# Optimization experiments

Measured on AMD Instinct MI355X. Metric: run time of the kernel, lower is better.

Reference implementation:

```python
import jax, jax.numpy as jnp
import numpy as np

CURVS = (-1.0, 0.0, 1.0, -0.5)
N, E, B = 50000, 800000, 128
IN, HID, OUT, GHID = 128, 128, 128, 32
K = len(CURVS)
TAU_MIN, TAU_MAX = 0.05, 10.0
EPS = 1e-15


def _vnorm(x):
    return jnp.maximum(jnp.linalg.norm(x, axis=-1, keepdims=True), EPS)


def tan_k(x, k):
    if k > 0:
        sk = np.sqrt(k)
        return jnp.tan(x * sk) / sk
    if k < 0:
        sk = np.sqrt(-k)
        return jnp.tanh(x * sk) / sk
    return x


def artan_k(x, k):
    if k > 0:
        sk = np.sqrt(k)
        return jnp.arctan(x * sk) / sk
    if k < 0:
        sk = np.sqrt(-k)
        return jnp.arctanh(jnp.clip(x * sk, -1.0 + 1e-7, 1.0 - 1e-7)) / sk
    return x


def project(x, k):
    # clip inside Poincare ball for k<0; identity otherwise (geoopt Stereographic.projx)
    if k < 0:
        maxn = (1.0 - 1e-5) / np.sqrt(-k)
        n = _vnorm(x)
        return jnp.where(n > maxn, x * (maxn / n), x)
    return x


def expmap0(u, k):
    n = _vnorm(u)
    return project(tan_k(n, k) * u / n, k)


def logmap0(y, k):
    n = _vnorm(y)
    return artan_k(n, k) * y / n


def mobius_add(x, y, k):
    x2 = jnp.sum(x * x, -1, keepdims=True)
    y2 = jnp.sum(y * y, -1, keepdims=True)
    xy = jnp.sum(x * y, -1, keepdims=True)
    num = (1.0 - 2.0 * k * xy - k * y2) * x + (1.0 + k * x2) * y
    den = jnp.maximum(1.0 - 2.0 * k * xy + k * k * x2 * y2, 1e-15)
    return project(num / den, k)


def mobius_matvec(W, x, k):
    mx = x @ W.T
    if k == 0:
        return mx
    xn = _vnorm(x)
    mxn = _vnorm(mx)
    res = tan_k(mxn / xn * artan_k(xn, k), k) * mx / mxn
    res = jnp.where(jnp.sum(jnp.abs(mx), -1, keepdims=True) == 0.0, 0.0, res)
    return project(res, k)


def dist(x, y, k):
    return 2.0 * artan_k(_vnorm(mobius_add(-x, y, k)), k)[..., 0]


def setup_inputs():
    key = jax.random.key(0)
    ks = jax.random.split(key, 12)
    x = jax.random.normal(ks[0], (N, IN), jnp.float32)
    edge_index = jax.random.randint(ks[1], (2, E), 0, N)
    batch = jnp.sort(jax.random.randint(ks[2], (N,), 0, B))
    s1 = float(np.sqrt(2.0 / (IN + HID)))
    s2 = float(np.sqrt(2.0 / (HID + OUT)))
    sg1 = float(np.sqrt(2.0 / (IN + GHID)))
    sg2 = float(np.sqrt(2.0 / (GHID + OUT)))
    raw0 = float(np.log(np.expm1(1.0 - TAU_MIN)))
    return {
        "x": x,
        "edge_index": edge_index,
        "batch": batch,
        "expert_w1": jax.random.normal(ks[3], (K, HID, IN), jnp.float32) * s1,
        "expert_b1": jnp.zeros((K, HID), jnp.float32),
        "expert_w2": jax.random.normal(ks[4], (K, OUT, HID), jnp.float32) * s2,
        "expert_b2": jnp.zeros((K, OUT), jnp.float32),
        "gate_w1": jax.random.normal(ks[5], (GHID, IN), jnp.float32) * sg1,
        "gate_b1": jnp.zeros((GHID,), jnp.float32),
        "gate_w2": jax.random.normal(ks[6], (OUT, GHID), jnp.float32) * sg2,
        "gate_b2": jnp.zeros((OUT,), jnp.float32),
        "gate_u": jax.random.normal(ks[7], (K, OUT), jnp.float32) * 0.02,
        "tau_raw": jnp.full((K,), raw0, jnp.float32),
    }


def _graph_norm(edge_index):
    loops = jnp.arange(N)
    row = jnp.concatenate([edge_index[0], loops])
    col = jnp.concatenate([edge_index[1], loops])
    deg = jax.ops.segment_sum(jnp.ones(E + N, jnp.float32), col, num_segments=N)
    dinv = deg ** -0.5  # deg >= 1 due to self loops
    return row, col, dinv[row] * dinv[col]


def _kappa_conv(xm, W, b, row, col, enorm, k):
    h = mobius_matvec(W, xm, k)
    bias_pt = expmap0(b[None, :], k)  # proju at origin is identity
    h = mobius_add(h, bias_pt, k)
    t = logmap0(h, k)  # [N, out]
    agg = jax.ops.segment_sum(enorm[:, None] * t[row], col, num_segments=N)
    return expmap0(agg, k)


def reference(x, edge_index, batch, expert_w1, expert_b1, expert_w2, expert_b2,
              gate_w1, gate_b1, gate_w2, gate_b2, gate_u, tau_raw):
    x = x.astype(jnp.float32)
    row, col, enorm = _graph_norm(edge_index)
    counts = jnp.maximum(
        jax.ops.segment_sum(jnp.ones(N, jnp.float32), batch, num_segments=B), 1.0)[:, None]

    # --- Riemannian experts ---
    embs = []
    for i, kv in enumerate(CURVS):
        xm = expmap0(x, kv)  # manifold init (proju at origin = identity)
        xm = _kappa_conv(xm, expert_w1[i], expert_b1[i], row, col, enorm, kv)
        xm = _kappa_conv(xm, expert_w2[i], expert_b2[i], row, col, enorm, kv)
        z = logmap0(xm, kv)
        embs.append(jax.ops.segment_sum(z, batch, num_segments=B) / counts)
    features = jnp.concatenate(embs, axis=-1)  # [B, K*OUT]

    # --- Euclidean gating encoder (GCN) ---
    def gcn(h, W, b):
        m = (h @ W.T)
        out = jax.ops.segment_sum(enorm[:, None] * m[row], col, num_segments=N) + b
        return jax.nn.relu(out)

    g = gcn(x, gate_w1, gate_b1)
    g = gcn(g, gate_w2, gate_b2)
    hgate = jax.ops.segment_sum(g, batch, num_segments=B) / counts  # [B, OUT]

    # --- Geometric distance gate ---
    tau = jnp.clip(jax.nn.softplus(tau_raw) + TAU_MIN, TAU_MIN, TAU_MAX)
    dists = []
    for i, kv in enumerate(CURVS):
        zk = expmap0(hgate, kv)
        yk = expmap0(gate_u[i][None, :], kv)
        dists.append(dist(zk, yk, kv))
    dists = jnp.stack(dists, axis=-1)  # [B, K]
    weights = jax.nn.softmax(-dists / tau[None, :], axis=-1)

    scaled = features * jnp.repeat(weights, OUT, axis=1)
    return scaled, weights, dists, tau
```

## Files before the change

### kernel.cpp

```cpp
#include <hip/hip_runtime.h>
#include <math.h>

#define NN 50000
#define EE 800000
#define ETOT (EE + NN)
#define BB 128
#define DIM 128
#define GHID 32
#define CHUNK 128
#define NCHUNK ((ETOT + CHUNK - 1) / CHUNK)
#define SCB 196

typedef _Float16 f16;
typedef _Float16 f16x2 __attribute__((ext_vector_type(2)));
typedef _Float16 f16x8 __attribute__((ext_vector_type(8)));
typedef float f32x4 __attribute__((ext_vector_type(4)));

struct CurvPack {
  float k[4], sk[4], mx[4];
};

__device__ __forceinline__ float wsum64(float v) {
#pragma unroll
  for (int m = 32; m; m >>= 1) v += __shfl_xor(v, m, 64);
  return v;
}

__device__ __forceinline__ float tan_k_d(float x, float kv, float sk) {
  if (kv > 0.f) return tanf(x * sk) / sk;
  if (kv < 0.f) return tanhf(x * sk) / sk;
  return x;
}

__device__ __forceinline__ float artan_k_d(float x, float kv, float sk) {
  if (kv > 0.f) return atanf(x * sk) / sk;
  if (kv < 0.f) {
    float t = x * sk;
    t = fminf(fmaxf(t, -1.f + 1e-7f), 1.f - 1e-7f);
    return atanhf(t) / sk;
  }
  return x;
}

__device__ __forceinline__ float proj_scale_d(float n, float kv, float maxn) {
  if (kv < 0.f && n > maxn) return maxn / n;
  return 1.f;
}

__global__ void k_init(float* __restrict__ deg, int n) {
  int i = blockIdx.x * 256 + threadIdx.x;
  if (i < n) deg[i] = 1.0f;
}

__global__ void k_counts(const int* __restrict__ batch, int* __restrict__ boff,
                         float* __restrict__ counts, int n) {
  int b = threadIdx.x;
  if (b <= 128) {
    int lo = 0, hi = n;
    while (lo < hi) {
      int mid = (lo + hi) >> 1;
      if (batch[mid] < b) lo = mid + 1; else hi = mid;
    }
    boff[b] = lo;
  }
  __syncthreads();
  if (b < 128) counts[b] = (float)(boff[b + 1] - boff[b]);
}

__global__ void k_deg(const int* __restrict__ ei, float* __restrict__ deg, int e) {
  int i = blockIdx.x * 256 + threadIdx.x;
  if (i < e) atomicAdd(&deg[ei[e + i]], 1.0f);
}

__global__ void k_dinv(float* __restrict__ deg, int* __restrict__ ideg, int n) {
  int i = blockIdx.x * 256 + threadIdx.x;
  if (i < n) {
    float d = deg[i];
    ideg[i] = (int)(d + 0.5f);
    deg[i] = 1.0f / sqrtf(d);
  }
}

__global__ void k_scanA(const int* __restrict__ ideg, int* __restrict__ bsum, int n) {
  __shared__ int ls[4];
  int i = blockIdx.x * 256 + threadIdx.x;
  int v = (i < n) ? ideg[i] : 0;
#pragma unroll
  for (int m = 1; m < 64; m <<= 1) v += __shfl_xor(v, m, 64);
  if ((threadIdx.x & 63) == 0) ls[threadIdx.x >> 6] = v;
  __syncthreads();
  if (threadIdx.x == 0) bsum[blockIdx.x] = ls[0] + ls[1] + ls[2] + ls[3];
}

__global__ void k_scanB(int* __restrict__ bsum, int nb) {
  __shared__ int wsh[4];
  int tid = threadIdx.x;
  int lane = tid & 63, w = tid >> 6;
  int v = (tid < nb) ? bsum[tid] : 0;
  int x = v;
#pragma unroll
  for (int o = 1; o < 64; o <<= 1) {
    int t = __shfl_up(x, o, 64);
    if (lane >= o) x += t;
  }
  if (lane == 63) wsh[w] = x;
  __syncthreads();
  int add = 0;
  for (int k2 = 0; k2 < w; k2++) add += wsh[k2];
  if (tid < nb) bsum[tid] = add + x - v;
}

__global__ void k_scanC(const int* __restrict__ ideg, const int* __restrict__ bsum,
                        int* __restrict__ off, int* __restrict__ cursor, int n) {
  __shared__ int wsh[4];
  int i = blockIdx.x * 256 + threadIdx.x;
  int lane = threadIdx.x & 63, w = threadIdx.x >> 6;
  int v = (i < n) ? ideg[i] : 0;
  int x = v;
#pragma unroll
  for (int o = 1; o < 64; o <<= 1) {
    int t = __shfl_up(x, o, 64);
    if (lane >= o) x += t;
  }
  if (lane == 63) wsh[w] = x;
  __syncthreads();
  int add = bsum[blockIdx.x];
  for (int k2 = 0; k2 < w; k2++) add += wsh[k2];
  int excl = add + x - v;
  if (i < n) {
    off[i] = excl;
    cursor[i] = excl;
  }
  if (i == n - 1) off[n] = excl + v;
}

__global__ void k_bnodes(const int* __restrict__ off, int* __restrict__ bnode, int nchunk,
                         int n) {
  int g = blockIdx.x * 256 + threadIdx.x;
  if (g >= nchunk) return;
  int e0 = g * CHUNK;
  int lo = 0, hi = n;
  while (hi - lo > 1) {
    int mid = (lo + hi) >> 1;
    if (off[mid] <= e0) lo = mid; else hi = mid;
  }
  bnode[g] = lo;
}

__global__ void k_bslot(const int* __restrict__ bnode, int* __restrict__ bslot, int nchunk) {
  int g = blockIdx.x * 256 + threadIdx.x;
  if (g >= nchunk) return;
  int v = bnode[g];
  int lo = 0, hi = g;
  while (lo < hi) {
    int mid = (lo + hi) >> 1;
    if (bnode[mid] < v) lo = mid + 1; else hi = mid;
  }
  bslot[g] = lo;
}

__device__ __forceinline__ bool span_head(const int* bnode, const int* bslot, const int* off,
                                          int g, int& nd) {
  if (bslot[g] != g) return false;
  nd = bnode[g];
  int s = off[nd], e = off[nd + 1];
  return (s / CHUNK) != ((e - 1) / CHUNK);
}

__global__ void k_zeroc(const int* __restrict__ bnode, const int* __restrict__ bslot,
                        const int* __restrict__ off, float* __restrict__ aggc, int nchunk) {
  int g = blockIdx.x * 4 + (threadIdx.x >> 6);
  int lane = threadIdx.x & 63;
  if (g >= nchunk) return;
  int nd;
  if (!span_head(bnode, bslot, off, g, nd)) return;
  float2 z = make_float2(0.f, 0.f);
#pragma unroll
  for (int i = 0; i < 4; i++) ((float2*)aggc)[(size_t)g * 256 + i * 64 + lane] = z;
}

__global__ void k_place(const int* __restrict__ ei, const float* __restrict__ dinv,
                        int* __restrict__ cursor, int2* __restrict__ esw, int e, int n) {
  int i = blockIdx.x * 256 + threadIdx.x;
  int et = e + n;
  if (i >= et) return;
  int r_, c_;
  if (i < e) {
    r_ = ei[i];
    c_ = ei[e + i];
  } else {
    r_ = i - e;
    c_ = i - e;
  }
  int p = atomicAdd(&cursor[c_], 1);
  esw[p] = make_int2(r_, __float_as_int(dinv[r_] * dinv[c_]));
}

__global__ void k_nodeprep(const float* __restrict__ x, float* __restrict__ scl,
                           float* __restrict__ xnk, int n, CurvPack cp) {
  int wid = blockIdx.x * 4 + (threadIdx.x >> 6);
  int lane = threadIdx.x & 63;
  if (wid >= n) return;
  float2 v = ((const float2*)x)[(size_t)wid * 64 + lane];
  float n2 = wsum64(v.x * v.x + v.y * v.y);
  float nraw = sqrtf(n2);
  if (lane < 4) {
    float kv = cp.k[lane], sk = cp.sk[lane], maxn = cp.mx[lane];
    float nnv = fmaxf(nraw, 1e-15f);
    float tk = tan_k_d(nnv, kv, sk);
    float s = tk / nnv;
    float pn = fmaxf(fabsf(tk) * (nraw / nnv), 1e-15f);
    float ps = proj_scale_d(pn, kv, maxn);
    scl[(size_t)lane * n + wid] = s * ps;
    xnk[(size_t)lane * n + wid] = pn * ps;
  }
}

__global__ void k_biaspt_all(const float* __restrict__ eb1, const float* __restrict__ eb2,
                             float* __restrict__ biasb, CurvPack cp) {
  __shared__ float l2[2];
  int blk = blockIdx.x;
  int ex = blk >> 1, layer = blk & 1;
  float kv = cp.k[ex], sk = cp.sk[ex], maxn = cp.mx[ex];
  const float* b = (layer ? eb2 : eb1) + ex * 128;
  float* outb = biasb + blk * 132;
  int j = threadIdx.x;
  float v = b[j];
  float n2 = wsum64(v * v);
  if ((j & 63) == 0) l2[j >> 6] = n2;
  __syncthreads();
  n2 = l2[0] + l2[1];
  float nraw = sqrtf(n2);
  float nnv = fmaxf(nraw, 1e-15f);
  float tk = tan_k_d(nnv, kv, sk);
  float s = tk / nnv;
  float pn = fmaxf(fabsf(tk) * (nraw / nnv), 1e-15f);
  float ps = proj_scale_d(pn, kv, maxn);
  float bp = ps * s * v;
  outb[j] = bp;
  float y2v = wsum64(bp * bp);
  __syncthreads();
  if ((j & 63) == 0) l2[j >> 6] = y2v;
  __syncthreads();
  if (j == 0) outb[128] = l2[0] + l2[1];
}

__global__ void k_w2h(const float* __restrict__ ew1, const float* __restrict__ ew2,
                      f16* __restrict__ whi, f16* __restrict__ wlo) {
  int i = blockIdx.x * 256 + threadIdx.x;
  if (i >= 8 * 16384) return;
  int slot = i >> 14;
  int r = i & 16383;
  int ex = slot >> 1, layer = slot & 1;
  float w = (layer ? ew2 : ew1)[ex * 16384 + r];
  f16 h = (f16)w;
  whi[i] = h;
  wlo[i] = (f16)(w - (float)h);
}

__global__ __launch_bounds__(256) void k_matmfma(
    const float* __restrict__ A, int astr, int aoffPerEx, const float* __restrict__ sclB,
    const float* __restrict__ xnkB, const f16* __restrict__ whiB,
    const f16* __restrict__ wloB, const float* __restrict__ biasB, int layer,
    f16* __restrict__ tout, int n, CurvPack cp) {
  __shared__ float red[3][16][4];
  __shared__ float redT[16][4];
  __shared__ float nAs[16], nCs[16], nL[16];
  int ex = blockIdx.y;
  float kv = cp.k[ex], sk = cp.sk[ex], maxn = cp.mx[ex];
  const f16* whi = whiB + (size_t)(ex * 2 + layer) * 16384;
  const f16* wlo = wloB + (size_t)(ex * 2 + layer) * 16384;
  const float* biasb = biasB + (ex * 2 + layer) * 132;
  const float* scale = sclB + (size_t)ex * n;
  const float* xnorm = xnkB + (size_t)ex * n;

  int tid = threadIdx.x;
  int w = tid >> 6;
  int lane = tid & 63;
  int col = lane & 15;
  int quad = lane >> 4;
  int n0w = blockIdx.x * 16;
  if (n0w >= n) return;

  int anodec = min(n0w + col, n - 1);
  const float* arow = A + (size_t)anodec * astr + ex * aoffPerEx;
  int jt0 = w * 2;

  f32x4 acc[2];
  acc[0] = (f32x4){0.f, 0.f, 0.f, 0.f};
  acc[1] = (f32x4){0.f, 0.f, 0.f, 0.f};

#pragma unroll
  for (int kc = 0; kc < 4; kc++) {
    int kb = kc * 32 + quad * 8;
    float4 a0 = *(const float4*)(arow + kb);
    float4 a1 = *(const float4*)(arow + kb + 4);
    float av[8] = {a0.x, a0.y, a0.z, a0.w, a1.x, a1.y, a1.z, a1.w};
    f16x8 Ah, Al;
#pragma unroll
    for (int i = 0; i < 8; i++) {
      f16 h = (f16)av[i];
      Ah[i] = h;
      Al[i] = (f16)(av[i] - (float)h);
    }
#pragma unroll
    for (int j2 = 0; j2 < 2; j2++) {
      const f16* bh = whi + (size_t)((jt0 + j2) * 16 + col) * 128 + kb;
      const f16* bl = wlo + (size_t)((jt0 + j2) * 16 + col) * 128 + kb;
      f16x8 Bh = *(const f16x8*)bh;
      f16x8 Bl = *(const f16x8*)bl;
      acc[j2] = __builtin_amdgcn_mfma_f32_16x16x32_f16(Ah, Bh, acc[j2], 0, 0, 0);
      acc[j2] = __builtin_amdgcn_mfma_f32_16x16x32_f16(Ah, Bl, acc[j2], 0, 0, 0);
      acc[j2] = __builtin_amdgcn_mfma_f32_16x16x32_f16(Al, Bh, acc[j2], 0, 0, 0);
    }
  }

  float bpj[2];
  bpj[0] = biasb[jt0 * 16 + col];
  bpj[1] = biasb[(jt0 + 1) * 16 + col];
  float y2 = biasb[128];

#pragma unroll
  for (int r = 0; r < 4; r++) {
    float s0 = 0.f, s1 = 0.f, s2 = 0.f;
#pragma unroll
    for (int j2 = 0; j2 < 2; j2++) {
      float v = acc[j2][r];
      s0 = fmaf(v, v, s0);
      s1 += fabsf(v);
      s2 = fmaf(v, bpj[j2], s2);
    }
#pragma unroll
    for (int m = 1; m < 16; m <<= 1) {
      s0 += __shfl_xor(s0, m, 64);
      s1 += __shfl_xor(s1, m, 64);
      s2 += __shfl_xor(s2, m, 64);
    }
    if (col == 0) {
      red[0][quad * 4 + r][w] = s0;
      red[1][quad * 4 + r][w] = s1;
      red[2][quad * 4 + r][w] = s2;
    }
  }
  __syncthreads();

  if (tid < 16) {
    int gnode = min(n0w + tid, n - 1);
    float sc = scale[gnode];
    float s0f = (red[0][tid][0] + red[0][tid][1] + red[0][tid][2] + red[0][tid][3]) * sc * sc;
    float s1f = (red[1][tid][0] + red[1][tid][1] + red[1][tid][2] + red[1][tid][3]) * fabsf(sc);
    float s2f = (red[2][tid][0] + red[2][tid][1] + red[2][tid][2] + red[2][tid][3]) * sc;
    float xnr = xnorm[gnode];
    float xn = fmaxf(xnr, 1e-15f);
    float mxraw = sqrtf(s0f);
    float mxv = fmaxf(mxraw, 1e-15f);
    float ar = artan_k_d(xn, kv, sk);
    float c1 = tan_k_d(mxv / xn * ar, kv, sk);
    float s = (s1f == 0.f) ? 0.f : c1 / mxv;
    float pn = fmaxf(fabsf(c1) * (mxraw / mxv), 1e-15f);
    float ps = (s1f == 0.f) ? 1.f : proj_scale_d(pn, kv, maxn);
    s *= ps;
    float x2 = (s * s) * s0f;
    float xy = s * s2f;
    float Aa = 1.f - 2.f * kv * xy - kv * y2;
    float Cc = 1.f + kv * x2;
    float den = fmaxf(1.f - 2.f * kv * xy + (kv * kv) * x2 * y2, 1e-15f);
    nAs[tid] = Aa * s / den * sc;
    nCs[tid] = Cc / den;
  }
  __syncthreads();

#pragma unroll
  for (int r = 0; r < 4; r++) {
    int idx = quad * 4 + r;
    float Asc = nAs[idx], Cs = nCs[idx];
    float t0 = 0.f;
#pragma unroll
    for (int j2 = 0; j2 < 2; j2++) {
      float v = fmaf(Asc, acc[j2][r], Cs * bpj[j2]);
      t0 = fmaf(v, v, t0);
    }
#pragma unroll
    for (int m = 1; m < 16; m <<= 1) t0 += __shfl_xor(t0, m, 64);
    if (col == 0) redT[idx][w] = t0;
  }
  __syncthreads();

  if (tid < 16) {
    float t0f = redT[tid][0] + redT[tid][1] + redT[tid][2] + redT[tid][3];
    float nraw = sqrtf(t0f);
    float ps2 = proj_scale_d(fmaxf(nraw, 1e-15f), kv, maxn);
    float nh = fmaxf(ps2 * nraw, 1e-15f);
    nL[tid] = artan_k_d(nh, kv, sk) / nh * ps2;
  }
  __syncthreads();

#pragma unroll
  for (int r = 0; r < 4; r++) {
    int idx = quad * 4 + r;
    int gnode = n0w + idx;
    if (gnode >= n) continue;
    float Asc = nAs[idx], Cs = nCs[idx], L = nL[idx];
    f16* trow = tout + (size_t)gnode * 512 + ex * 128;
#pragma unroll
    for (int j2 = 0; j2 < 2; j2++) {
      float v = fmaf(Asc, acc[j2][r], Cs * bpj[j2]);
      trow[(jt0 + j2) * 16 + col] = (f16)(L * v);
    }
  }
}

template <int MODE, int NE>
__global__ __launch_bounds__(256) void k_aggF(
    const int2* __restrict__ esw, const int* __restrict__ off,
    const int* __restrict__ bnode, const int* __restrict__ bslot,
    const int* __restrict__ batch, const f16x2* __restrict__ t, float* __restrict__ agg1,
    float* __restrict__ aggc, float* __restrict__ scl2, float* __restrict__ xnk2,
    float* __restrict__ feats, const float* __restrict__ bias, float* __restrict__ hgate,
    int etot, int n, CurvPack cp) {
  int gw = blockIdx.x * 4 + (threadIdx.x >> 6);
  int lane = threadIdx.x & 63;
  int e0 = gw * CHUNK;
  if (e0 >= etot) return;
  int e1 = min(e0 + CHUNK, etot);
  int bnHead = bnode[gw];
  int slotA = bslot[gw];
  int slotB = ((gw + 1) * CHUNK < etot) ? bslot[gw + 1] : slotA;
  int cur = bnHead;
  int runStart = off[cur];
  int eend = off[cur + 1];
  float ax[NE], ay[NE], pax[NE], pay[NE];
#pragma unroll
  for (int e = 0; e < NE; e++) {
    ax[e] = ay[e] = pax[e] = pay[e] = 0.f;
  }
  int bcur = (MODE >= 1) ? batch[cur] : 0;
  float bbx = 0.f, bby = 0.f;
  if (MODE == 2) {
    float2 bb = ((const float2*)bias)[lane];
    bbx = bb.x;
    bby = bb.y;
  }

  auto flushInterior = [&]() {
#pragma unroll
    for (int e = 0; e < NE; e++) {
      if (MODE == 0) {
        ((float2*)agg1)[(size_t)cur * 256 + e * 64 + lane] = make_float2(ax[e], ay[e]);
        float n2 = wsum64(fmaf(ax[e], ax[e], ay[e] * ay[e]));
        float nraw = sqrtf(n2);
        float nnv = fmaxf(nraw, 1e-15f);
        float tk = tan_k_d(nnv, cp.k[e], cp.sk[e]);
        float s = tk / nnv;
        float pn = fmaxf(fabsf(tk) * (nraw / nnv), 1e-15f);
        float ps = proj_scale_d(pn, cp.k[e], cp.mx[e]);
        if (lane == 0) {
          scl2[(size_t)e * n + cur] = s * ps;
          xnk2[(size_t)e * n + cur] = pn * ps;
        }
      } else if (MODE == 1) {
        float n2 = wsum64(fmaf(ax[e], ax[e], ay[e] * ay[e]));
        float nraw = sqrtf(n2);
        float nnv = fmaxf(nraw, 1e-15f);
        float tk = tan_k_d(nnv, cp.k[e], cp.sk[e]);
        float s = tk / nnv;
        float pn = fmaxf(fabsf(tk) * (nraw / nnv), 1e-15f);
        float ps = proj_scale_d(pn, cp.k[e], cp.mx[e]);
        s *= ps;
        float nh = fmaxf(pn * ps, 1e-15f);
        float sc = artan_k_d(nh, cp.k[e], cp.sk[e]) / nh * s;
        pax[e] = fmaf(sc, ax[e], pax[e]);
        pay[e] = fmaf(sc, ay[e], pay[e]);
      } else {
        pax[e] += fmaxf(ax[e] + bbx, 0.f);
        pay[e] += fmaxf(ay[e] + bby, 0.f);
      }
    }
  };
  auto flushBoundary = [&]() {
    int slot = (cur == bnHead) ? slotA : slotB;
#pragma unroll
    for (int e = 0; e < NE; e++) {
      float* dp = aggc + (size_t)slot * 512 + e * 128 + lane * 2;
      atomicAdd(dp, ax[e]);
      atomicAdd(dp + 1, ay[e]);
    }
  };
  auto flushPool = [&]() {
#pragma unroll
    for (int e = 0; e < NE; e++) {
      if (MODE == 1) {
        float* fp = &feats[(size_t)bcur * 512 + e * 128 + lane * 2];
        atomicAdd(fp, pax[e]);
        atomicAdd(fp + 1, pay[e]);
      } else if (MODE == 2) {
        float* hp = &hgate[(size_t)bcur * 128 + lane * 2];
        atomicAdd(hp, pax[e]);
        atomicAdd(hp + 1, pay[e]);
      }
    }
  };

  int j = e0;
  while (j < e1) {
    if (j + 8 <= e1 && eend >= j + 8) {
      int2 m[8];
#pragma unroll
      for (int q = 0; q < 8; q++) m[q] = esw[j + q];
      f16x2 r[8][NE];
#pragma unroll
      for (int q = 0; q < 8; q++) {
        int s = __builtin_amdgcn_readfirstlane(m[q].x);
        const f16x2* base = t + (size_t)s * 256;
#pragma unroll
        for (int e = 0; e < NE; e++) r[q][e] = base[e * 64 + lane];
      }
#pragma unroll
      for (int q = 0; q < 8; q++) {
        float w = __int_as_float(m[q].y);
#pragma unroll
        for (int e = 0; e < NE; e++) {
          ax[e] = fmaf(w, (float)r[q][e][0], ax[e]);
          ay[e] = fmaf(w, (float)r[q][e][1], ay[e]);
        }
      }
      j += 8;
    } else if (j + 4 <= e1 && eend >= j + 4) {
      int2 m[4];
#pragma unroll
      for (int q = 0; q < 4; q++) m[q] = esw[j + q];
      f16x2 r[4][NE];
#pragma unroll
      for (int q = 0; q < 4; q++) {
        int s = __builtin_amdgcn_readfirstlane(m[q].x);
        const f16x2* base = t + (size_t)s * 256;
#pragma unroll
        for (int e = 0; e < NE; e++) r[q][e] = base[e * 64 + lane];
      }
#pragma unroll
      for (int q = 0; q < 4; q++) {
        float w = __int_as_float(m[q].y);
#pragma unroll
        for (int e = 0; e < NE; e++) {
          ax[e] = fmaf(w, (float)r[q][e][0], ax[e]);
          ay[e] = fmaf(w, (float)r[q][e][1], ay[e]);
        }
      }
      j += 4;
    } else {
      if (j == eend) {
        if (runStart >= e0) flushInterior(); else flushBoundary();
#pragma unroll
        for (int e = 0; e < NE; e++) ax[e] = ay[e] = 0.f;
        runStart = j;
        cur++;
        eend = off[cur + 1];
        if (MODE >= 1) {
          int nb = batch[cur];
          if (nb != bcur) {
            flushPool();
#pragma unroll
            for (int e = 0; e < NE; e++) pax[e] = pay[e] = 0.f;
            bcur = nb;
          }
        }
      }
      int2 m = esw[j];
      int s = __builtin_amdgcn_readfirstlane(m.x);
      const f16x2* base = t + (size_t)s * 256;
      float w = __int_as_float(m.y);
#pragma unroll
      for (int e = 0; e < NE; e++) {
        f16x2 rv = base[e * 64 + lane];
        ax[e] = fmaf(w, (float)rv[0], ax[e]);
        ay[e] = fmaf(w, (float)rv[1], ay[e]);
      }
      j++;
    }
  }
  if (runStart >= e0 && eend <= e1) flushInterior(); else flushBoundary();
  if (MODE >= 1) flushPool();
}

__global__ void k_fix1(const int* __restrict__ bnode, const int* __restrict__ bslot,
                       const int* __restrict__ off, const float* __restrict__ aggc,
                       float* __restrict__ agg1, float* __restrict__ scl2,
                       float* __restrict__ xnk2, int nchunk, int n, CurvPack cp) {
  int g = blockIdx.x * 4 + (threadIdx.x >> 6);
  int lane = threadIdx.x & 63;
  if (g >= nchunk) return;
  int nd;
  if (!span_head(bnode, bslot, off, g, nd)) return;
#pragma unroll
  for (int e = 0; e < 4; e++) {
    float2 v = ((const float2*)aggc)[(size_t)g * 256 + e * 64 + lane];
    ((float2*)agg1)[(size_t)nd * 256 + e * 64 + lane] = v;
    float n2 = wsum64(fmaf(v.x, v.x, v.y * v.y));
    float nraw = sqrtf(n2);
    float nnv = fmaxf(nraw, 1e-15f);
    float tk = tan_k_d(nnv, cp.k[e], cp.sk[e]);
    float s = tk / nnv;
    float pn = fmaxf(fabsf(tk) * (nraw / nnv), 1e-15f);
    float ps = proj_scale_d(pn, cp.k[e], cp.mx[e]);
    if (lane == 0) {
      scl2[(size_t)e * n + nd] = s * ps;
      xnk2[(size_t)e * n + nd] = pn * ps;
    }
  }
}

__global__ void k_fix2(const int* __restrict__ bnode, const int* __restrict__ bslot,
                       const int* __restrict__ off, const float* __restrict__ aggc,
                       const int* __restrict__ batch, float* __restrict__ feats, int nchunk,
                       CurvPack cp) {
  int g = blockIdx.x * 4 + (threadIdx.x >> 6);
  int lane = threadIdx.x & 63;
  if (g >= nchunk) return;
  int nd;
  if (!span_head(bnode, bslot, off, g, nd)) return;
  int b = batch[nd];
#pragma unroll
  for (int e = 0; e < 4; e++) {
    float2 v = ((const float2*)aggc)[(size_t)g * 256 + e * 64 + lane];
    float n2 = wsum64(fmaf(v.x, v.x, v.y * v.y));
    float nraw = sqrtf(n2);
    float nnv = fmaxf(nraw, 1e-15f);
    float tk = tan_k_d(nnv, cp.k[e], cp.sk[e]);
    float s = tk / nnv;
    float pn = fmaxf(fabsf(tk) * (nraw / nnv), 1e-15f);
    float ps = proj_scale_d(pn, cp.k[e], cp.mx[e]);
    s *= ps;
    float nh = fmaxf(pn * ps, 1e-15f);
    float sc = artan_k_d(nh, cp.k[e], cp.sk[e]) / nh * s;
    float* fp = &feats[(size_t)b * 512 + e * 128 + lane * 2];
    atomicAdd(fp, sc * v.x);
    atomicAdd(fp + 1, sc * v.y);
  }
}

__global__ void k_fixG(const int* __restrict__ bnode, const int* __restrict__ bslot,
                       const int* __restrict__ off, const float* __restrict__ aggc,
                       const int* __restrict__ batch, const float* __restrict__ bias,
                       float* __restrict__ hgate, int nchunk) {
  int g = blockIdx.x * 4 + (threadIdx.x >> 6);
  int lane = threadIdx.x & 63;
  if (g >= nchunk) return;
  int nd;
  if (!span_head(bnode, bslot, off, g, nd)) return;
  float2 v = ((const float2*)aggc)[(size_t)g * 256 + lane];
  float2 bb = ((const float2*)bias)[lane];
  int b = batch[nd];
  float* hp = &hgate[(size_t)b * 128 + lane * 2];
  atomicAdd(hp, fmaxf(v.x + bb.x, 0.f));
  atomicAdd(hp + 1, fmaxf(v.y + bb.y, 0.f));
}

__global__ __launch_bounds__(256) void k_gate1(const float* __restrict__ x,
                                               const float* __restrict__ gw1,
                                               float* __restrict__ m1, int n) {
  __shared__ float xT[64][68];
  __shared__ float Wt[64][36];
  int tid = threadIdx.x;
  int n0 = blockIdx.x * 64;
  int c = tid & 7, r = tid >> 3;
  float acc[2][4];
#pragma unroll
  for (int i = 0; i < 2; i++)
#pragma unroll
    for (int jj = 0; jj < 4; jj++) acc[i][jj] = 0.f;

  for (int kc = 0; kc < 2; kc++) {
    if (kc) __syncthreads();
#pragma unroll
    for (int it = 0; it < 8; it++) {
      int u = tid + it * 256;
      int j = u >> 6, kd = u & 63;
      Wt[kd][j] = gw1[j * 128 + kc * 64 + kd];
    }
#pragma unroll
    for (int it = 0; it < 4; it++) {
      int u = tid + it * 256;
      int node = u >> 4, c4 = u & 15;
      float4 v = make_float4(0.f, 0.f, 0.f, 0.f);
      if (n0 + node < n) v = ((const float4*)x)[(size_t)(n0 + node) * 32 + kc * 16 + c4];
      xT[4 * c4 + 0][node] = v.x;
      xT[4 * c4 + 1][node] = v.y;
      xT[4 * c4 + 2][node] = v.z;
      xT[4 * c4 + 3][node] = v.w;
    }
    __syncthreads();
#pragma unroll 8
    for (int kd = 0; kd < 64; kd++) {
      float2 av = *(const float2*)&xT[kd][r * 2];
      float4 bv = *(const float4*)&Wt[kd][c * 4];
      float a[2] = {av.x, av.y};
      float bbv[4] = {bv.x, bv.y, bv.z, bv.w};
#pragma unroll
      for (int i = 0; i < 2; i++)
#pragma unroll
        for (int jj = 0; jj < 4; jj++) acc[i][jj] = fmaf(a[i], bbv[jj], acc[i][jj]);
    }
  }
#pragma unroll
  for (int i = 0; i < 2; i++) {
    int node = n0 + r * 2 + i;
    if (node >= n) continue;
    ((float4*)m1)[(size_t)node * 8 + c] = make_float4(acc[i][0], acc[i][1], acc[i][2], acc[i][3]);
  }
}

__global__ __launch_bounds__(256) void k_gate2(const float* __restrict__ g1,
                                               const float* __restrict__ gw2,
                                               f16* __restrict__ m2, int n) {
  __shared__ float xT[32][68];
  __shared__ float Wt[32][132];
  int tid = threadIdx.x;
  int n0 = blockIdx.x * 64;
  int c = tid & 15, r = tid >> 4;
  float acc[4][8];
#pragma unroll
  for (int i = 0; i < 4; i++)
#pragma unroll
    for (int jj = 0; jj < 8; jj++) acc[i][jj] = 0.f;

#pragma unroll
  for (int it = 0; it < 16; it++) {
    int u = tid + it * 256;
    int j = u >> 5, kd = u & 31;
    Wt[kd][j] = gw2[j * 32 + kd];
  }
#pragma unroll
  for (int it = 0; it < 2; it++) {
    int u = tid + it * 256;
    int node = u >> 3, c4 = u & 7;
    float4 v = make_float4(0.f, 0.f, 0.f, 0.f);
    if (n0 + node < n) v = ((const float4*)g1)[(size_t)(n0 + node) * 8 + c4];
    xT[4 * c4 + 0][node] = v.x;
    xT[4 * c4 + 1][node] = v.y;
    xT[4 * c4 + 2][node] = v.z;
    xT[4 * c4 + 3][node] = v.w;
  }
  __syncthreads();
#pragma unroll 8
  for (int kd = 0; kd < 32; kd++) {
    float4 av = *(const float4*)&xT[kd][r * 4];
    float4 b0 = *(const float4*)&Wt[kd][c * 8];
    float4 b1 = *(const float4*)&Wt[kd][c * 8 + 4];
    float a[4] = {av.x, av.y, av.z, av.w};
    float bbv[8] = {b0.x, b0.y, b0.z, b0.w, b1.x, b1.y, b1.z, b1.w};
#pragma unroll
    for (int i = 0; i < 4; i++)
#pragma unroll
      for (int jj = 0; jj < 8; jj++) acc[i][jj] = fmaf(a[i], bbv[jj], acc[i][jj]);
  }
#pragma unroll
  for (int i = 0; i < 4; i++) {
    int node = n0 + r * 4 + i;
    if (node >= n) continue;
    f16x8 hv;
#pragma unroll
    for (int jj = 0; jj < 8; jj++) hv[jj] = (f16)acc[i][jj];
    *((f16x8*)(m2 + (size_t)node * 512) + c) = hv;
  }
}

__global__ void k_agg_relu32(const float* __restrict__ m1, const int* __restrict__ off,
                             const int2* __restrict__ esw, const float* __restrict__ bias,
                             float* __restrict__ g1, int n) {
  int node = blockIdx.x * 4 + (threadIdx.x >> 6);
  int lane = threadIdx.x & 63;
  if (node >= n) return;
  int grp = lane >> 3, l8 = lane & 7;
  int e0 = off[node], e1 = off[node + 1];
  float4 acc = make_float4(0.f, 0.f, 0.f, 0.f);
  for (int base = e0 + grp; base < e1; base += 8) {
    int2 me = esw[base];
    int ss = me.x;
    float ww = __int_as_float(me.y);
    float4 tv = ((const float4*)m1)[(size_t)ss * 8 + l8];
    acc.x = fmaf(ww, tv.x, acc.x);
    acc.y = fmaf(ww, tv.y, acc.y);
    acc.z = fmaf(ww, tv.z, acc.z);
    acc.w = fmaf(ww, tv.w, acc.w);
  }
#pragma unroll
  for (int m = 8; m <= 32; m <<= 1) {
    acc.x += __shfl_xor(acc.x, m, 64);
    acc.y += __shfl_xor(acc.y, m, 64);
    acc.z += __shfl_xor(acc.z, m, 64);
    acc.w += __shfl_xor(acc.w, m, 64);
  }
  if (grp == 0) {
    float4 bb = ((const float4*)bias)[l8];
    float4 o = make_float4(fmaxf(acc.x + bb.x, 0.f), fmaxf(acc.y + bb.y, 0.f),
                           fmaxf(acc.z + bb.z, 0.f), fmaxf(acc.w + bb.w, 0.f));
    ((float4*)g1)[(size_t)node * 8 + l8] = o;
  }
}

__global__ __launch_bounds__(128) void k_final(const float* __restrict__ feats,
                                               const float* __restrict__ hgate,
                                               const float* __restrict__ counts,
                                               const float* __restrict__ gate_u,
                                               const float* __restrict__ tau_raw,
                                               float* __restrict__ out, CurvPack cp) {
  __shared__ float l2[2];
  int b = blockIdx.x;
  int j = threadIdx.x;
  float cnt = fmaxf(counts[b], 1.f);
  float hg = hgate[(size_t)b * 128 + j] / cnt;

  auto bsum = [&](float v) -> float {
    v = wsum64(v);
    __syncthreads();
    if ((j & 63) == 0) l2[j >> 6] = v;
    __syncthreads();
    return l2[0] + l2[1];
  };

  float nhg2 = bsum(hg * hg);
  float nhgraw = sqrtf(nhg2);
  float nhg = fmaxf(nhgraw, 1e-15f);

  float d[4], tau[4];
#pragma unroll
  for (int i = 0; i < 4; i++) {
    float kv = cp.k[i], sk = cp.sk[i], mxn = cp.mx[i];
    float tk = tan_k_d(nhg, kv, sk);
    float s = tk / nhg;
    float pn = fmaxf(fabsf(tk) * (nhgraw / nhg), 1e-15f);
    s *= proj_scale_d(pn, kv, mxn);
    float zk = s * hg;

    float u = gate_u[i * 128 + j];
    float nu2 = bsum(u * u);
    float nuraw = sqrtf(nu2);
    float nu = fmaxf(nuraw, 1e-15f);
    float tku = tan_k_d(nu, kv, sk);
    float su = tku / nu;
    float pnu = fmaxf(fabsf(tku) * (nuraw / nu), 1e-15f);
    su *= proj_scale_d(pnu, kv, mxn);
    float yk = su * u;

    float xv = -zk;
    float x2 = bsum(xv * xv);
    float y2 = bsum(yk * yk);
    float xy = bsum(xv * yk);
    float A = 1.f - 2.f * kv * xy - kv * y2;
    float C = 1.f + kv * x2;
    float den = fmaxf(1.f - 2.f * kv * xy + (kv * kv) * x2 * y2, 1e-15f);
    float ma = (A * xv + C * yk) / den;
    float m2 = bsum(ma * ma);
    float mraw = sqrtf(m2);
    float ps2 = proj_scale_d(fmaxf(mraw, 1e-15f), kv, mxn);
    float nm = fmaxf(ps2 * mraw, 1e-15f);
    d[i] = 2.f * artan_k_d(nm, kv, sk);

    float tr = tau_raw[i];
    tau[i] = fminf(fmaxf(log1pf(expf(tr)) + 0.05f, 0.05f), 10.f);
  }

  float xi[4];
  float mxv = -1e30f;
#pragma unroll
  for (int i = 0; i < 4; i++) {
    xi[i] = -d[i] / tau[i];
    mxv = fmaxf(mxv, xi[i]);
  }
  float es = 0.f, e[4];
#pragma unroll
  for (int i = 0; i < 4; i++) {
    e[i] = expf(xi[i] - mxv);
    es += e[i];
  }
  float w[4];
#pragma unroll
  for (int i = 0; i < 4; i++) w[i] = e[i] / es;

#pragma unroll
  for (int i = 0; i < 4; i++)
    out[(size_t)b * 512 + i * 128 + j] = feats[(size_t)b * 512 + i * 128 + j] / cnt * w[i];

  if (j < 4) {
    out[65536 + b * 4 + j] = w[j];
    out[66048 + b * 4 + j] = d[j];
  }
  if (b == 0 && j < 4) out[66560 + j] = tau[j];
}

extern "C" void kernel_launch(void* const* d_in, const int* in_sizes, int n_in,
                              void* d_out, int out_size, void* d_ws, size_t ws_size,
                              hipStream_t stream) {
  const float* x = (const float*)d_in[0];
  const int* ei = (const int*)d_in[1];
  const int* batch = (const int*)d_in[2];
  const float* ew1 = (const float*)d_in[3];
  const float* eb1 = (const float*)d_in[4];
  const float* ew2 = (const float*)d_in[5];
  const float* eb2 = (const float*)d_in[6];
  const float* gw1 = (const float*)d_in[7];
  const float* gb1 = (const float*)d_in[8];
  const float* gw2 = (const float*)d_in[9];
  const float* gb2 = (const float*)d_in[10];
  const float* gu = (const float*)d_in[11];
  const float* traw = (const float*)d_in[12];
  float* out = (float*)d_out;

  const int N = NN, E = EE, ET = ETOT, B = BB;

  float* ws = (float*)d_ws;
  size_t o = 0;
  f16* t4 = (f16*)ws;       o += (size_t)N * 256;
  float* agg1 = ws + o;     o += (size_t)N * 512;
  float* aggc = ws + o;     o += (size_t)NCHUNK * 512;
  float* deg = ws + o;      o += N;
  float* scl1 = ws + o;     o += (size_t)4 * N;
  float* xnk1 = ws + o;     o += (size_t)4 * N;
  float* scl2 = ws + o;     o += (size_t)4 * N;
  float* xnk2 = ws + o;     o += (size_t)4 * N;
  float* counts = ws + o;   o += 256;
  float* feats = ws + o;    o += (size_t)B * 512;
  float* hg = ws + o;       o += (size_t)B * 128;
  float* biasb = ws + o;    o += 8 * 132;
  f16* whi = (f16*)(ws + o);    o += 8 * 16384 / 2;
  f16* wlo = (f16*)(ws + o);    o += 8 * 16384 / 2;
  int* ideg = (int*)(ws + o);   o += N;
  int* csroff = (int*)(ws + o); o += N + 8;
  int* cursor = (int*)(ws + o); o += N;
  int* boff = (int*)(ws + o);   o += 136;
  int* bsum = (int*)(ws + o);   o += 256;
  int* bnode = (int*)(ws + o);  o += NCHUNK + 8;
  int* bslot = (int*)(ws + o);  o += NCHUNK + 8;
  int2* esw = (int2*)(ws + o);  o += (size_t)2 * ET;

  float* m1 = agg1;
  float* g1 = agg1 + (size_t)N * 32;

  hipMemsetAsync(counts, 0, (256 + (size_t)B * 512 + (size_t)B * 128) * sizeof(float), stream);

  const double curvs[4] = {-1.0, 0.0, 1.0, -0.5};
  CurvPack cp;
  for (int i = 0; i < 4; i++) {
    double kd = curvs[i];
    double skd = sqrt(fabs(kd));
    cp.k[i] = (float)kd;
    cp.sk[i] = (float)skd;
    cp.mx[i] = (kd < 0) ? (float)((1.0 - 1e-5) / skd) : 3.0e38f;
  }

  k_init<<<(N + 255) / 256, 256, 0, stream>>>(deg, N);
  k_counts<<<1, 256, 0, stream>>>(batch, boff, counts, N);
  k_deg<<<(E + 255) / 256, 256, 0, stream>>>(ei, deg, E);
  k_dinv<<<(N + 255) / 256, 256, 0, stream>>>(deg, ideg, N);
  k_scanA<<<SCB, 256, 0, stream>>>(ideg, bsum, N);
  k_scanB<<<1, 256, 0, stream>>>(bsum, SCB);
  k_scanC<<<SCB, 256, 0, stream>>>(ideg, bsum, csroff, cursor, N);
  k_bnodes<<<(NCHUNK + 255) / 256, 256, 0, stream>>>(csroff, bnode, NCHUNK, N);
  k_bslot<<<(NCHUNK + 255) / 256, 256, 0, stream>>>(bnode, bslot, NCHUNK);
  k_place<<<(ET + 255) / 256, 256, 0, stream>>>(ei, deg, cursor, esw, E, N);
  k_nodeprep<<<(N + 3) / 4, 256, 0, stream>>>(x, scl1, xnk1, N, cp);
  k_biaspt_all<<<8, 128, 0, stream>>>(eb1, eb2, biasb, cp);
  k_w2h<<<512, 256, 0, stream>>>(ew1, ew2, whi, wlo);

  const int aggBlocks = (NCHUNK + 3) / 4;
  dim3 mfmaGrid((N + 15) / 16, 4);

  k_matmfma<<<mfmaGrid, 256, 0, stream>>>(x, 128, 0, scl1, xnk1, whi, wlo, biasb, 0, t4, N, cp);
  k_zeroc<<<aggBlocks, 256, 0, stream>>>(bnode, bslot, csroff, aggc, NCHUNK);
  k_aggF<0, 4><<<aggBlocks, 256, 0, stream>>>(esw, csroff, bnode, bslot, batch,
                                              (const f16x2*)t4, agg1, aggc, scl2, xnk2, nullptr,
                                              nullptr, nullptr, ET, N, cp);
  k_fix1<<<aggBlocks, 256, 0, stream>>>(bnode, bslot, csroff, aggc, agg1, scl2, xnk2, NCHUNK, N,
                                        cp);
  k_matmfma<<<mfmaGrid, 256, 0, stream>>>(agg1, 512, 128, scl2, xnk2, whi, wlo, biasb, 1, t4, N,
                                          cp);
  k_zeroc<<<aggBlocks, 256, 0, stream>>>(bnode, bslot, csroff, aggc, NCHUNK);
  k_aggF<1, 4><<<aggBlocks, 256, 0, stream>>>(esw, csroff, bnode, bslot, batch,
                                              (const f16x2*)t4, nullptr, aggc, nullptr, nullptr,
                                              feats, nullptr, nullptr, ET, N, cp);
  k_fix2<<<aggBlocks, 256, 0, stream>>>(bnode, bslot, csroff, aggc, batch, feats, NCHUNK, cp);

  k_gate1<<<(N + 63) / 64, 256, 0, stream>>>(x, gw1, m1, N);
  k_agg_relu32<<<(N + 3) / 4, 256, 0, stream>>>(m1, csroff, esw, gb1, g1, N);
  k_gate2<<<(N + 63) / 64, 256, 0, stream>>>(g1, gw2, t4, N);
  k_zeroc<<<aggBlocks, 256, 0, stream>>>(bnode, bslot, csroff, aggc, NCHUNK);
  k_aggF<2, 1><<<aggBlocks, 256, 0, stream>>>(esw, csroff, bnode, bslot, batch,
                                              (const f16x2*)t4, nullptr, aggc, nullptr, nullptr,
                                              nullptr, gb2, hg, ET, N, cp);
  k_fixG<<<aggBlocks, 256, 0, stream>>>(bnode, bslot, csroff, aggc, batch, gb2, hg, NCHUNK);

  k_final<<<B, 128, 0, stream>>>(feats, hg, counts, gu, traw, out, cp);

  (void)in_sizes; (void)n_in; (void)out_size; (void)ws_size;
}
```

Before: 1.024 ms.

## Store expert messages in FP8 E4M3 and accumulate gathers in half2

The per-node transformed expert features are now written as FP8 E4M3 in an interleaved layout, so each lane fetches one 8-byte word covering all four experts per edge. The aggregation kernels decode with packed fp8-to-half conversion and accumulate with half2 FMAs. Together these halve the gather traffic of the memory-bound edge aggregation and cut ALU work. The gate aggregation moves into its own specialised kernel with a compact f16 layout. FP8 storage and fp16 accumulation add significant rounding and overflow risk and may break the accuracy tolerance.

Measured after the change: 1.442 ms. 1.41x slower.

```diff
diff --git a/kernel.cpp b/kernel.cpp
--- a/kernel.cpp
+++ b/kernel.cpp
@@ -1,4 +1,6 @@
 #include <hip/hip_runtime.h>
+#include <hip/hip_fp16.h>
+#include <hip/hip_fp8.h>
 #include <math.h>
 
 #define NN 50000
@@ -45,6 +47,16 @@
 __device__ __forceinline__ float proj_scale_d(float n, float kv, float maxn) {
   if (kv < 0.f && n > maxn) return maxn / n;
   return 1.f;
+}
+
+__device__ __forceinline__ unsigned char enc8(float x) {
+  return (unsigned char)__hip_cvt_float_to_fp8(x, __HIP_SATFINITE, __HIP_E4M3);
+}
+__device__ __forceinline__ __half2 dec2(unsigned short v) {
+  __half2_raw r2 = __hip_cvt_fp8x2_to_halfraw2((__hip_fp8x2_storage_t)v, __HIP_E4M3);
+  union { __half2_raw r; __half2 h; } u;
+  u.r = r2;
+  return u.h;
 }
 
 __global__ void k_init(float* __restrict__ deg, int n) {
@@ -262,7 +274,7 @@
     const float* __restrict__ A, int astr, int aoffPerEx, const float* __restrict__ sclB,
     const float* __restrict__ xnkB, const f16* __restrict__ whiB,
     const f16* __restrict__ wloB, const float* __restrict__ biasB, int layer,
-    f16* __restrict__ tout, int n, CurvPack cp) {
+    unsigned char* __restrict__ tout, int n, CurvPack cp) {
   __shared__ float red[3][16][4];
   __shared__ float redT[16][4];
   __shared__ float nAs[16], nCs[16], nL[16];
@@ -401,23 +413,23 @@
     int gnode = n0w + idx;
     if (gnode >= n) continue;
     float Asc = nAs[idx], Cs = nCs[idx], L = nL[idx];
-    f16* trow = tout + (size_t)gnode * 512 + ex * 128;
+    unsigned char* trow = tout + (size_t)gnode * 512;
 #pragma unroll
     for (int j2 = 0; j2 < 2; j2++) {
       float v = fmaf(Asc, acc[j2][r], Cs * bpj[j2]);
-      trow[(jt0 + j2) * 16 + col] = (f16)(L * v);
-    }
-  }
-}
-
-template <int MODE, int NE>
+      int d = (jt0 + j2) * 16 + col;
+      trow[(d >> 1) * 8 + ex * 2 + (d & 1)] = enc8(L * v);
+    }
+  }
+}
+
+template <int MODE>
 __global__ __launch_bounds__(256) void k_aggF(
     const int2* __restrict__ esw, const int* __restrict__ off,
     const int* __restrict__ bnode, const int* __restrict__ bslot,
-    const int* __restrict__ batch, const f16x2* __restrict__ t, float* __restrict__ agg1,
-    float* __restrict__ aggc, float* __restrict__ scl2, float* __restrict__ xnk2,
-    float* __restrict__ feats, const float* __restrict__ bias, float* __restrict__ hgate,
-    int etot, int n, CurvPack cp) {
+    const int* __restrict__ batch, const unsigned char* __restrict__ t8,
+    float* __restrict__ agg1, float* __restrict__ aggc, float* __restrict__ scl2,
+    float* __restrict__ xnk2, float* __restrict__ feats, int etot, int n, CurvPack cp) {
   int gw = blockIdx.x * 4 + (threadIdx.x >> 6);
   int lane = threadIdx.x & 63;
   int e0 = gw * CHUNK;
@@ -429,25 +441,22 @@
   int cur = bnHead;
   int runStart = off[cur];
   int eend = off[cur + 1];
-  float ax[NE], ay[NE], pax[NE], pay[NE];
-#pragma unroll
-  for (int e = 0; e < NE; e++) {
-    ax[e] = ay[e] = pax[e] = pay[e] = 0.f;
-  }
-  int bcur = (MODE >= 1) ? batch[cur] : 0;
-  float bbx = 0.f, bby = 0.f;
-  if (MODE == 2) {
-    float2 bb = ((const float2*)bias)[lane];
-    bbx = bb.x;
-    bby = bb.y;
-  }
+  __half2 hz = __half2half2(__float2half(0.f));
+  __half2 axh[4];
+#pragma unroll
+  for (int e = 0; e < 4; e++) axh[e] = hz;
+  float pax[4], pay[4];
+#pragma unroll
+  for (int e = 0; e < 4; e++) pax[e] = pay[e] = 0.f;
+  int bcur = (MODE == 1) ? batch[cur] : 0;
 
   auto flushInterior = [&]() {
 #pragma unroll
-    for (int e = 0; e < NE; e++) {
+    for (int e = 0; e < 4; e++) {
+      float2 f = __half22float2(axh[e]);
       if (MODE == 0) {
-        ((float2*)agg1)[(size_t)cur * 256 + e * 64 + lane] = make_float2(ax[e], ay[e]);
-        float n2 = wsum64(fmaf(ax[e], ax[e], ay[e] * ay[e]));
+        ((float2*)agg1)[(size_t)cur * 256 + e * 64 + lane] = f;
+        float n2 = wsum64(fmaf(f.x, f.x, f.y * f.y));
         float nraw = sqrtf(n2);
         float nnv = fmaxf(nraw, 1e-15f);
         float tk = tan_k_d(nnv, cp.k[e], cp.sk[e]);
@@ -458,8 +467,8 @@
           scl2[(size_t)e * n + cur] = s * ps;
           xnk2[(size_t)e * n + cur] = pn * ps;
         }
-      } else if (MODE == 1) {
-        float n2 = wsum64(fmaf(ax[e], ax[e], ay[e] * ay[e]));
+      } else {
+        float n2 = wsum64(fmaf(f.x, f.x, f.y * f.y));
         float nraw = sqrtf(n2);
         float nnv = fmaxf(nraw, 1e-15f);
         float tk = tan_k_d(nnv, cp.k[e], cp.sk[e]);
@@ -469,34 +478,28 @@
         s *= ps;
         float nh = fmaxf(pn * ps, 1e-15f);
         float sc = artan_k_d(nh, cp.k[e], cp.sk[e]) / nh * s;
-        pax[e] = fmaf(sc, ax[e], pax[e]);
-        pay[e] = fmaf(sc, ay[e], pay[e]);
-      } else {
-        pax[e] += fmaxf(ax[e] + bbx, 0.f);
-        pay[e] += fmaxf(ay[e] + bby, 0.f);
+        pax[e] = fmaf(sc, f.x, pax[e]);
+        pay[e] = fmaf(sc, f.y, pay[e]);
       }
     }
   };
   auto flushBoundary = [&]() {
     int slot = (cur == bnHead) ? slotA : slotB;
 #pragma unroll
-    for (int e = 0; e < NE; e++) {
+    for (int e = 0; e < 4; e++) {
+      float2 f = __half22float2(axh[e]);
       float* dp = aggc + (size_t)slot * 512 + e * 128 + lane * 2;
-      atomicAdd(dp, ax[e]);
-      atomicAdd(dp + 1, ay[e]);
+      atomicAdd(dp, f.x);
+      atomicAdd(dp + 1, f.y);
     }
   };
   auto flushPool = [&]() {
-#pragma unroll
-    for (int e = 0; e < NE; e++) {
-      if (MODE == 1) {
+    if (MODE == 1) {
+#pragma unroll
+      for (int e = 0; e < 4; e++) {
         float* fp = &feats[(size_t)bcur * 512 + e * 128 + lane * 2];
         atomicAdd(fp, pax[e]);
         atomicAdd(fp + 1, pay[e]);
-      } else if (MODE == 2) {
-        float* hp = &hgate[(size_t)bcur * 128 + lane * 2];
-        atomicAdd(hp, pax[e]);
-        atomicAdd(hp + 1, pay[e]);
       }
     }
   };
@@ -507,79 +510,170 @@
       int2 m[8];
 #pragma unroll
       for (int q = 0; q < 8; q++) m[q] = esw[j + q];
-      f16x2 r[8][NE];
+      uint2 rv[8];
 #pragma unroll
       for (int q = 0; q < 8; q++) {
         int s = __builtin_amdgcn_readfirstlane(m[q].x);
-        const f16x2* base = t + (size_t)s * 256;
-#pragma unroll
-        for (int e = 0; e < NE; e++) r[q][e] = base[e * 64 + lane];
+        rv[q] = *(const uint2*)(t8 + (size_t)s * 512 + lane * 8);
       }
 #pragma unroll
       for (int q = 0; q < 8; q++) {
-        float w = __int_as_float(m[q].y);
-#pragma unroll
-        for (int e = 0; e < NE; e++) {
-          ax[e] = fmaf(w, (float)r[q][e][0], ax[e]);
-          ay[e] = fmaf(w, (float)r[q][e][1], ay[e]);
-        }
+        __half2 wh = __half2half2(__float2half(__int_as_float(m[q].y)));
+        axh[0] = __hfma2(wh, dec2((unsigned short)(rv[q].x & 0xffff)), axh[0]);
+        axh[1] = __hfma2(wh, dec2((unsigned short)(rv[q].x >> 16)), axh[1]);
+        axh[2] = __hfma2(wh, dec2((unsigned short)(rv[q].y & 0xffff)), axh[2]);
+        axh[3] = __hfma2(wh, dec2((unsigned short)(rv[q].y >> 16)), axh[3]);
       }
       j += 8;
     } else if (j + 4 <= e1 && eend >= j + 4) {
       int2 m[4];
 #pragma unroll
       for (int q = 0; q < 4; q++) m[q] = esw[j + q];
-      f16x2 r[4][NE];
+      uint2 rv[4];
 #pragma unroll
       for (int q = 0; q < 4; q++) {
         int s = __builtin_amdgcn_readfirstlane(m[q].x);
-        const f16x2* base = t + (size_t)s * 256;
-#pragma unroll
-        for (int e = 0; e < NE; e++) r[q][e] = base[e * 64 + lane];
+        rv[q] = *(const uint2*)(t8 + (size_t)s * 512 + lane * 8);
       }
 #pragma unroll
       for (int q = 0; q < 4; q++) {
-        float w = __int_as_float(m[q].y);
-#pragma unroll
-        for (int e = 0; e < NE; e++) {
-          ax[e] = fmaf(w, (float)r[q][e][0], ax[e]);
-          ay[e] = fmaf(w, (float)r[q][e][1], ay[e]);
-        }
+        __half2 wh = __half2half2(__float2half(__int_as_float(m[q].y)));
+        axh[0] = __hfma2(wh, dec2((unsigned short)(rv[q].x & 0xffff)), axh[0]);
+        axh[1] = __hfma2(wh, dec2((unsigned short)(rv[q].x >> 16)), axh[1]);
+        axh[2] = __hfma2(wh, dec2((unsigned short)(rv[q].y & 0xffff)), axh[2]);
+        axh[3] = __hfma2(wh, dec2((unsigned short)(rv[q].y >> 16)), axh[3]);
       }
       j += 4;
     } else {
       if (j == eend) {
         if (runStart >= e0) flushInterior(); else flushBoundary();
 #pragma unroll
-        for (int e = 0; e < NE; e++) ax[e] = ay[e] = 0.f;
+        for (int e = 0; e < 4; e++) axh[e] = hz;
         runStart = j;
         cur++;
         eend = off[cur + 1];
-        if (MODE >= 1) {
+        if (MODE == 1) {
           int nb = batch[cur];
           if (nb != bcur) {
             flushPool();
 #pragma unroll
-            for (int e = 0; e < NE; e++) pax[e] = pay[e] = 0.f;
+            for (int e = 0; e < 4; e++) pax[e] = pay[e] = 0.f;
             bcur = nb;
           }
         }
       }
       int2 m = esw[j];
       int s = __builtin_amdgcn_readfirstlane(m.x);
-      const f16x2* base = t + (size_t)s * 256;
+      uint2 rv = *(const uint2*)(t8 + (size_t)s * 512 + lane * 8);
+      __half2 wh = __half2half2(__float2half(__int_as_float(m.y)));
+      axh[0] = __hfma2(wh, dec2((unsigned short)(rv.x & 0xffff)), axh[0]);
+      axh[1] = __hfma2(wh, dec2((unsigned short)(rv.x >> 16)), axh[1]);
+      axh[2] = __hfma2(wh, dec2((unsigned short)(rv.y & 0xffff)), axh[2]);
+      axh[3] = __hfma2(wh, dec2((unsigned short)(rv.y >> 16)), axh[3]);
+      j++;
+    }
+  }
+  if (runStart >= e0 && eend <= e1) flushInterior(); else flushBoundary();
+  if (MODE == 1) flushPool();
+}
+
+__global__ __launch_bounds__(256) void k_aggG(
+    const int2* __restrict__ esw, const int* __restrict__ off,
+    const int* __restrict__ bnode, const int* __restrict__ bslot,
+    const int* __restrict__ batch, const f16x2* __restrict__ t, float* __restrict__ aggc,
+    const float* __restrict__ bias, float* __restrict__ hgate, int etot, int n) {
+  int gw = blockIdx.x * 4 + (threadIdx.x >> 6);
+  int lane = threadIdx.x & 63;
+  int e0 = gw * CHUNK;
+  if (e0 >= etot) return;
+  int e1 = min(e0 + CHUNK, etot);
+  int bnHead = bnode[gw];
+  int slotA = bslot[gw];
+  int slotB = ((gw + 1) * CHUNK < etot) ? bslot[gw + 1] : slotA;
+  int cur = bnHead;
+  int runStart = off[cur];
+  int eend = off[cur + 1];
+  float ax = 0.f, ay = 0.f, pax = 0.f, pay = 0.f;
+  int bcur = batch[cur];
+  float2 bb = ((const float2*)bias)[lane];
+
+  auto flushInterior = [&]() {
+    pax += fmaxf(ax + bb.x, 0.f);
+    pay += fmaxf(ay + bb.y, 0.f);
+  };
+  auto flushBoundary = [&]() {
+    int slot = (cur == bnHead) ? slotA : slotB;
+    float* dp = aggc + (size_t)slot * 512 + lane * 2;
+    atomicAdd(dp, ax);
+    atomicAdd(dp + 1, ay);
+  };
+  auto flushPool = [&]() {
+    float* hp = &hgate[(size_t)bcur * 128 + lane * 2];
+    atomicAdd(hp, pax);
+    atomicAdd(hp + 1, pay);
+  };
+
+  int j = e0;
+  while (j < e1) {
+    if (j + 8 <= e1 && eend >= j + 8) {
+      int2 m[8];
+#pragma unroll
+      for (int q = 0; q < 8; q++) m[q] = esw[j + q];
+      f16x2 r[8];
+#pragma unroll
+      for (int q = 0; q < 8; q++) {
+        int s = __builtin_amdgcn_readfirstlane(m[q].x);
+        r[q] = t[(size_t)s * 64 + lane];
+      }
+#pragma unroll
+      for (int q = 0; q < 8; q++) {
+        float w = __int_as_float(m[q].y);
+        ax = fmaf(w, (float)r[q][0], ax);
+        ay = fmaf(w, (float)r[q][1], ay);
+      }
+      j += 8;
+    } else if (j + 4 <= e1 && eend >= j + 4) {
+      int2 m[4];
+#pragma unroll
+      for (int q = 0; q < 4; q++) m[q] = esw[j + q];
+      f16x2 r[4];
+#pragma unroll
+      for (int q = 0; q < 4; q++) {
+        int s = __builtin_amdgcn_readfirstlane(m[q].x);
+        r[q] = t[(size_t)s * 64 + lane];
+      }
+#pragma unroll
+      for (int q = 0; q < 4; q++) {
+        float w = __int_as_float(m[q].y);
+        ax = fmaf(w, (float)r[q][0], ax);
+        ay = fmaf(w, (float)r[q][1], ay);
+      }
+      j += 4;
+    } else {
+      if (j == eend) {
+        if (runStart >= e0) flushInterior(); else flushBoundary();
+        ax = ay = 0.f;
+        runStart = j;
+        cur++;
+        eend = off[cur + 1];
+        int nb = batch[cur];
+        if (nb != bcur) {
+          flushPool();
+          pax = pay = 0.f;
+          bcur = nb;
+        }
+      }
+      int2 m = esw[j];
+      int s = __builtin_amdgcn_readfirstlane(m.x);
+      f16x2 rv = t[(size_t)s * 64 + lane];
       float w = __int_as_float(m.y);
-#pragma unroll
-      for (int e = 0; e < NE; e++) {
-        f16x2 rv = base[e * 64 + lane];
-        ax[e] = fmaf(w, (float)rv[0], ax[e]);
-        ay[e] = fmaf(w, (float)rv[1], ay[e]);
-      }
+      ax = fmaf(w, (float)rv[0], ax);
+      ay = fmaf(w, (float)rv[1], ay);
       j++;
     }
   }
   if (runStart >= e0 && eend <= e1) flushInterior(); else flushBoundary();
-  if (MODE >= 1) flushPool();
+  flushPool();
 }
 
 __global__ void k_fix1(const int* __restrict__ bnode, const int* __restrict__ bslot,
@@ -760,7 +854,7 @@
     f16x8 hv;
 #pragma unroll
     for (int jj = 0; jj < 8; jj++) hv[jj] = (f16)acc[i][jj];
-    *((f16x8*)(m2 + (size_t)node * 512) + c) = hv;
+    *((f16x8*)(m2 + (size_t)node * 128) + c) = hv;
   }
 }
 
@@ -910,7 +1004,7 @@
 
   float* ws = (float*)d_ws;
   size_t o = 0;
-  f16* t4 = (f16*)ws;       o += (size_t)N * 256;
+  unsigned char* t8 = (unsigned char*)ws;  o += (size_t)N * 128;
   float* agg1 = ws + o;     o += (size_t)N * 512;
   float* aggc = ws + o;     o += (size_t)NCHUNK * 512;
   float* deg = ws + o;      o += N;
@@ -935,6 +1029,7 @@
 
   float* m1 = agg1;
   float* g1 = agg1 + (size_t)N * 32;
+  f16* tg = (f16*)t8;
 
   hipMemsetAsync(counts, 0, (256 + (size_t)B * 512 + (size_t)B * 128) * sizeof(float), stream);
 
@@ -965,28 +1060,25 @@
   const int aggBlocks = (NCHUNK + 3) / 4;
   dim3 mfmaGrid((N + 15) / 16, 4);
 
-  k_matmfma<<<mfmaGrid, 256, 0, stream>>>(x, 128, 0, scl1, xnk1, whi, wlo, biasb, 0, t4, N, cp);
+  k_matmfma<<<mfmaGrid, 256, 0, stream>>>(x, 128, 0, scl1, xnk1, whi, wlo, biasb, 0, t8, N, cp);
   k_zeroc<<<aggBlocks, 256, 0, stream>>>(bnode, bslot, csroff, aggc, NCHUNK);
-  k_aggF<0, 4><<<aggBlocks, 256, 0, stream>>>(esw, csroff, bnode, bslot, batch,
-                                              (const f16x2*)t4, agg1, aggc, scl2, xnk2, nullptr,
-                                              nullptr, nullptr, ET, N, cp);
+  k_aggF<0><<<aggBlocks, 256, 0, stream>>>(esw, csroff, bnode, bslot, batch, t8, agg1, aggc,
+                                           scl2, xnk2, nullptr, ET, N, cp);
   k_fix1<<<aggBlocks, 256, 0, stream>>>(bnode, bslot, csroff, aggc, agg1, scl2, xnk2, NCHUNK, N,
                                         cp);
-  k_matmfma<<<mfmaGrid, 256, 0, stream>>>(agg1, 512, 128, scl2, xnk2, whi, wlo, biasb, 1, t4, N,
+  k_matmfma<<<mfmaGrid, 256, 0, stream>>>(agg1, 512, 128, scl2, xnk2, whi, wlo, biasb, 1, t8, N,
                                           cp);
   k_zeroc<<<aggBlocks, 256, 0, stream>>>(bnode, bslot, csroff, aggc, NCHUNK);
-  k_aggF<1, 4><<<aggBlocks, 256, 0, stream>>>(esw, csroff, bnode, bslot, batch,
-                                              (const f16x2*)t4, nullptr, aggc, nullptr, nullptr,
-                                              feats, nullptr, nullptr, ET, N, cp);
+  k_aggF<1><<<aggBlocks, 256, 0, stream>>>(esw, csroff, bnode, bslot, batch, t8, nullptr, aggc,
+                                           nullptr, nullptr, feats, ET, N, cp);
   k_fix2<<<aggBlocks, 256, 0, stream>>>(bnode, bslot, csroff, aggc, batch, feats, NCHUNK, cp);
 
   k_gate1<<<(N + 63) / 64, 256, 0, stream>>>(x, gw1, m1, N);
   k_agg_relu32<<<(N + 3) / 4, 256, 0, stream>>>(m1, csroff, esw, gb1, g1, N);
-  k_gate2<<<(N + 63) / 64, 256, 0, stream>>>(g1, gw2, t4, N);
+  k_gate2<<<(N + 63) / 64, 256, 0, stream>>>(g1, gw2, tg, N);
   k_zeroc<<<aggBlocks, 256, 0, stream>>>(bnode, bslot, csroff, aggc, NCHUNK);
-  k_aggF<2, 1><<<aggBlocks, 256, 0, stream>>>(esw, csroff, bnode, bslot, batch,
-                                              (const f16x2*)t4, nullptr, aggc, nullptr, nullptr,
-                                              nullptr, gb2, hg, ET, N, cp);
+  k_aggG<<<aggBlocks, 256, 0, stream>>>(esw, csroff, bnode, bslot, batch, (const f16x2*)tg,
+                                        aggc, gb2, hg, ET, N);
   k_fixG<<<aggBlocks, 256, 0, stream>>>(bnode, bslot, csroff, aggc, batch, gb2, hg, NCHUNK);
 
   k_final<<<B, 128, 0, stream>>>(feats, hg, counts, gu, traw, out, cp);
```
